# Kernel tuning notes

Measured on AMD Instinct MI355X. Metric: run time of the kernel, lower is better.

The kernel has to match this reference:

```python
import jax, jax.numpy as jnp
import numpy as np

B, S, D, H = 4, 2048, 1024, 16
DK = D // H


def setup_inputs() -> dict:
    key = jax.random.key(0)
    ks = jax.random.split(key, 12)
    s = 1.0 / np.sqrt(D)
    inp = {
        "query": jax.random.normal(ks[0], (B, S, D), jnp.float32),
        "key": jax.random.normal(ks[1], (B, S, D), jnp.float32),
        "value": jax.random.normal(ks[2], (B, S, D), jnp.float32),
        "mask": jax.random.randint(ks[3], (B, S, S), 0, 2, jnp.int32),
        "Wq": jax.random.uniform(ks[4], (D, D), jnp.float32, -s, s),
        "bq": jax.random.uniform(ks[5], (D,), jnp.float32, -s, s),
        "Wk": jax.random.uniform(ks[6], (D, D), jnp.float32, -s, s),
        "bk": jax.random.uniform(ks[7], (D,), jnp.float32, -s, s),
        "Wv": jax.random.uniform(ks[8], (D, D), jnp.float32, -s, s),
        "bv": jax.random.uniform(ks[9], (D,), jnp.float32, -s, s),
        "Wo": jax.random.uniform(ks[10], (D, D), jnp.float32, -s, s),
        "bo": jax.random.uniform(ks[11], (D,), jnp.float32, -s, s),
    }
    return inp


def reference(query, key, value, mask, Wq, bq, Wk, bk, Wv, bv, Wo, bo):
    # Linear projections (torch Linear: x @ W.T + b), split into heads: [B,H,S,DK]
    def proj(x, W, b):
        y = x @ W.T + b
        return y.reshape(B, S, H, DK).transpose(0, 2, 1, 3)

    q = proj(query, Wq, bq)
    k = proj(key, Wk, bk)
    v = proj(value, Wv, bv)

    # scores: [B,H,S,S]
    scores = jnp.einsum("bhqd,bhkd->bhqk", q, k) / jnp.sqrt(jnp.float32(DK))
    m = mask[:, None, :, :]  # broadcast over heads
    scores = jnp.where(m == 0, jnp.float32(-1e9), scores)
    attn = jax.nn.softmax(scores, axis=-1)
    out = jnp.einsum("bhqk,bhkd->bhqd", attn, v)
    out = out.transpose(0, 2, 1, 3).reshape(B, S, D)
    return out @ Wo.T + bo
```

## Files before the change

### kernel.cpp

```cpp
#include <hip/hip_runtime.h>

#define B_  4
#define S_  2048
#define D_  1024
#define H_  16
#define DK_ 64

typedef __attribute__((ext_vector_type(8))) __bf16 bf16x8;
typedef __attribute__((ext_vector_type(4))) float  f32x4;

#define AS1 __attribute__((address_space(1)))
#define AS3 __attribute__((address_space(3)))

__device__ __forceinline__ void gl2lds16(const void* g, void* l) {
    __builtin_amdgcn_global_load_lds((const AS1 unsigned int*)g,
                                     (AS3 unsigned int*)l, 16, 0, 0);
}

__device__ __forceinline__ unsigned short f2bf(float f) {
    union { float f; unsigned u; } v; v.f = f;
    return (unsigned short)((v.u + 0x7FFFu + ((v.u >> 16) & 1u)) >> 16);
}

__device__ __forceinline__ unsigned pk_bf16(float f0, float f1) {
    union { float f; unsigned u; } a, b; a.f = f0; b.f = f1;
    return __builtin_amdgcn_perm(b.u + 0x8000u, a.u + 0x8000u, 0x07060302u);
}

__device__ __forceinline__ void cast8(const float* __restrict__ x,
                                      unsigned short* __restrict__ y, int i) {
    float4 a = ((const float4*)x)[2 * i];
    float4 b = ((const float4*)x)[2 * i + 1];
    uint4 w;
    w.x = pk_bf16(a.x, a.y);
    w.y = pk_bf16(a.z, a.w);
    w.z = pk_bf16(b.x, b.y);
    w.w = pk_bf16(b.z, b.w);
    ((uint4*)y)[i] = w;
}

__global__ __launch_bounds__(256) void cast_act(
    const float* __restrict__ a, const float* __restrict__ b,
    const float* __restrict__ c, unsigned short* __restrict__ ya,
    unsigned short* __restrict__ yb, unsigned short* __restrict__ yc)
{
    const int sel = blockIdx.y;
    const float* x = (sel == 0) ? a : (sel == 1) ? b : c;
    unsigned short* y = (sel == 0) ? ya : (sel == 1) ? yb : yc;
    cast8(x, y, blockIdx.x * 256 + threadIdx.x);
}

__global__ __launch_bounds__(256) void cast_w(
    const float* __restrict__ a, const float* __restrict__ b,
    const float* __restrict__ c, const float* __restrict__ d,
    unsigned short* __restrict__ ya, unsigned short* __restrict__ yb,
    unsigned short* __restrict__ yc, unsigned short* __restrict__ yd)
{
    const int sel = blockIdx.y;
    const float* x = (sel == 0) ? a : (sel == 1) ? b : (sel == 2) ? c : d;
    unsigned short* y = (sel == 0) ? ya : (sel == 1) ? yb : (sel == 2) ? yc : yd;
    cast8(x, y, blockIdx.x * 256 + threadIdx.x);
}

__global__ __launch_bounds__(256, 3) void gemm_qkv(
    const unsigned short* __restrict__ Xq, const unsigned short* __restrict__ Xk,
    const unsigned short* __restrict__ Xv, const unsigned short* __restrict__ Wqkv,
    const float* __restrict__ bq, const float* __restrict__ bk,
    const float* __restrict__ bv, unsigned short* __restrict__ Qw,
    unsigned short* __restrict__ Kw, unsigned short* __restrict__ Vt,
    float qscale)
{
    __shared__ unsigned short As[128 * 64];
    __shared__ unsigned short Bs[128 * 64];

    const int tid  = threadIdx.x;
    const int lane = tid & 63, wave = tid >> 6;
    const int l16  = lane & 15, quad = lane >> 4;
    const int wm = wave & 1, wn = wave >> 1;
    const int n0 = blockIdx.x * 128, m0 = blockIdx.y * 128;
    const int xr = l16 & 7;

    const int sel = blockIdx.x >> 3;
    const unsigned short* X = (sel == 0) ? Xq : (sel == 1) ? Xk : Xv;

    const int row8 = lane >> 3;
    const int sc   = ((lane & 7) ^ row8) * 8;

    f32x4 acc[4][4] = {};

    for (int k0 = 0; k0 < D_; k0 += 64) {
        __syncthreads();
        #pragma unroll
        for (int j = 0; j < 4; ++j) {
            const int ca = wave * 4 + j;
            const int r  = ca * 8 + row8;
            gl2lds16(X    + (size_t)(m0 + r) * D_ + k0 + sc, &As[ca * 512 + (lane & 63) * 8]);
            gl2lds16(Wqkv + (size_t)(n0 + r) * D_ + k0 + sc, &Bs[ca * 512 + (lane & 63) * 8]);
        }
        __syncthreads();

        #pragma unroll
        for (int s = 0; s < 2; ++s) {
            bf16x8 a[4], bb[4];
            #pragma unroll
            for (int i = 0; i < 4; ++i)
                a[i] = *(const bf16x8*)&As[(wm * 64 + i * 16 + l16) * 64 + (((s * 4 + quad) ^ xr)) * 8];
            #pragma unroll
            for (int j = 0; j < 4; ++j)
                bb[j] = *(const bf16x8*)&Bs[(wn * 64 + j * 16 + l16) * 64 + (((s * 4 + quad) ^ xr)) * 8];
            #pragma unroll
            for (int i = 0; i < 4; ++i)
                #pragma unroll
                for (int j = 0; j < 4; ++j)
                    acc[i][j] = __builtin_amdgcn_mfma_f32_16x16x32_bf16(a[i], bb[j], acc[i][j], 0, 0, 0);
        }
    }

    const int ncol = (blockIdx.x & 7) * 128 + wn * 64;
    const float scale = (sel == 0) ? qscale : 1.0f;
    const float* bias = (sel == 0) ? bq : (sel == 1) ? bk : bv;

    if (sel == 2) {
        const int bb_ = m0 >> 11;
        #pragma unroll
        for (int j = 0; j < 4; ++j) {
            const int dk = ncol + j * 16 + l16;
            const float bvv = bias[dk];
            #pragma unroll
            for (int i = 0; i < 4; ++i) {
                const int sb = (m0 & (S_ - 1)) + wm * 64 + i * 16 + quad * 4;
                uint2 w;
                w.x = pk_bf16(acc[i][j][0] + bvv, acc[i][j][1] + bvv);
                w.y = pk_bf16(acc[i][j][2] + bvv, acc[i][j][3] + bvv);
                *(uint2*)(Vt + (size_t)(bb_ * D_ + dk) * S_ + sb) = w;
            }
        }
    } else {
        unsigned short* Outp = sel ? Kw : Qw;
        #pragma unroll
        for (int j = 0; j < 4; ++j) {
            const int n = ncol + j * 16 + l16;
            const float bvv = bias[n];
            #pragma unroll
            for (int i = 0; i < 4; ++i) {
                #pragma unroll
                for (int r = 0; r < 4; ++r) {
                    const int m = m0 + wm * 64 + i * 16 + quad * 4 + r;
                    Outp[(size_t)m * D_ + n] = f2bf((acc[i][j][r] + bvv) * scale);
                }
            }
        }
    }
}

__global__ __launch_bounds__(256, 3) void gemm_out(
    const unsigned short* __restrict__ X, const unsigned short* __restrict__ W,
    const float* __restrict__ bias, float* __restrict__ Out)
{
    __shared__ unsigned short As[128 * 64];
    __shared__ unsigned short Bs[128 * 64];

    const int tid  = threadIdx.x;
    const int lane = tid & 63, wave = tid >> 6;
    const int l16  = lane & 15, quad = lane >> 4;
    const int wm = wave & 1, wn = wave >> 1;
    const int n0 = blockIdx.x * 128, m0 = blockIdx.y * 128;
    const int xr = l16 & 7;

    const int row8 = lane >> 3;
    const int sc   = ((lane & 7) ^ row8) * 8;

    f32x4 acc[4][4] = {};

    for (int k0 = 0; k0 < D_; k0 += 64) {
        __syncthreads();
        #pragma unroll
        for (int j = 0; j < 4; ++j) {
            const int ca = wave * 4 + j;
            const int r  = ca * 8 + row8;
            gl2lds16(X + (size_t)(m0 + r) * D_ + k0 + sc, &As[ca * 512 + (lane & 63) * 8]);
            gl2lds16(W + (size_t)(n0 + r) * D_ + k0 + sc, &Bs[ca * 512 + (lane & 63) * 8]);
        }
        __syncthreads();

        #pragma unroll
        for (int s = 0; s < 2; ++s) {
            bf16x8 a[4], bb[4];
            #pragma unroll
            for (int i = 0; i < 4; ++i)
                a[i] = *(const bf16x8*)&As[(wm * 64 + i * 16 + l16) * 64 + (((s * 4 + quad) ^ xr)) * 8];
            #pragma unroll
            for (int j = 0; j < 4; ++j)
                bb[j] = *(const bf16x8*)&Bs[(wn * 64 + j * 16 + l16) * 64 + (((s * 4 + quad) ^ xr)) * 8];
            #pragma unroll
            for (int i = 0; i < 4; ++i)
                #pragma unroll
                for (int j = 0; j < 4; ++j)
                    acc[i][j] = __builtin_amdgcn_mfma_f32_16x16x32_bf16(a[i], bb[j], acc[i][j], 0, 0, 0);
        }
    }

    #pragma unroll
    for (int j = 0; j < 4; ++j) {
        const int n = n0 + wn * 64 + j * 16 + l16;
        const float bv = bias[n];
        #pragma unroll
        for (int i = 0; i < 4; ++i) {
            #pragma unroll
            for (int r = 0; r < 4; ++r) {
                const int m = m0 + wm * 64 + i * 16 + quad * 4 + r;
                Out[(size_t)m * D_ + n] = acc[i][j][r] + bv;
            }
        }
    }
}

__global__ __launch_bounds__(256) void pack_mask(
    const int* __restrict__ mask, unsigned long long* __restrict__ pm)
{
    const int gid  = blockIdx.x * 256 + threadIdx.x;
    const int w    = gid >> 6;
    const int lane = threadIdx.x & 63;
    const int mv = mask[(size_t)w * 64 + lane];
    const unsigned long long bal = __ballot(mv != 0);
    if (lane == 0) pm[w] = bal;
}

__global__ __launch_bounds__(256, 4) void attn_kernel(
    const unsigned short* __restrict__ Q,
    const unsigned short* __restrict__ Kg,
    const unsigned short* __restrict__ Vt,
    const unsigned long long* __restrict__ pm,
    unsigned short* __restrict__ O)
{
    __shared__ unsigned short Ks[64 * 64];
    __shared__ unsigned short VsT[80 * 64];
    __shared__ unsigned short Ps[64 * 72];

    const int tid  = threadIdx.x;
    const int lane = tid & 63, wave = tid >> 6;
    const int l16  = lane & 15, quad = lane >> 4;
    const int bh = blockIdx.y, b = bh >> 4, h = bh & 15;
    const int q0 = blockIdx.x * 64;
    const int xq = l16 & 7;

    {
        uint2 ones; ones.x = 0x3F803F80u; ones.y = 0x3F803F80u;
        *(uint2*)&VsT[64 * 64 + tid * 4] = ones;
    }

    bf16x8 qa[2];
    {
        const unsigned short* qp =
            Q + (size_t)(b * S_ + q0 + wave * 16 + l16) * D_ + h * DK_ + quad * 8;
        qa[0] = *(const bf16x8*)qp;
        qa[1] = *(const bf16x8*)(qp + 32);
    }

    const unsigned long long* pmq =
        pm + (size_t)(b * S_ + q0 + wave * 16 + l16) * (S_ / 64);

    f32x4 oacc[5] = {};

    for (int kt = 0; kt < S_ / 64; ++kt) {
        const int k0 = kt * 64;
        __syncthreads();
        #pragma unroll
        for (int j = 0; j < 2; ++j) {
            const int c = j * 256 + tid;
            const int row = c >> 3;
            const int cl = (c & 7) ^ (row & 7);
            gl2lds16(Kg + (size_t)(b * S_ + k0 + row) * D_ + h * DK_ + cl * 8, &Ks[c * 8]);
            gl2lds16(Vt + (size_t)(b * D_ + h * DK_ + row) * S_ + k0 + cl * 8, &VsT[c * 8]);
        }
        __syncthreads();

        f32x4 sct[4] = {};
        #pragma unroll
        for (int s = 0; s < 2; ++s) {
            const int cs = ((s * 4 + quad) ^ xq) * 8;
            #pragma unroll
            for (int mb = 0; mb < 4; ++mb) {
                bf16x8 ka = *(const bf16x8*)&Ks[(mb * 16 + l16) * 64 + cs];
                sct[mb] = __builtin_amdgcn_mfma_f32_16x16x32_bf16(ka, qa[s], sct[mb], 0, 0, 0);
            }
        }

        const unsigned long long wq = pmq[kt];
        #pragma unroll
        for (int mb = 0; mb < 4; ++mb) {
            const unsigned nib = (unsigned)(wq >> (mb * 16 + quad * 4)) & 0xFu;
            float e[4];
            #pragma unroll
            for (int r = 0; r < 4; ++r) {
                float x = __builtin_amdgcn_exp2f(sct[mb][r]);
                e[r] = ((nib >> r) & 1u) ? x : 0.f;
            }
            uint2 w;
            w.x = pk_bf16(e[0], e[1]);
            w.y = pk_bf16(e[2], e[3]);
            *(uint2*)&Ps[(wave * 16 + l16) * 72 + mb * 16 + quad * 4] = w;
        }

        #pragma unroll
        for (int s = 0; s < 2; ++s) {
            bf16x8 pa = *(const bf16x8*)&Ps[(wave * 16 + l16) * 72 + s * 32 + quad * 8];
            const int cs = ((s * 4 + quad) ^ xq) * 8;
            #pragma unroll
            for (int db = 0; db < 5; ++db) {
                bf16x8 vb = *(const bf16x8*)&VsT[(db * 16 + l16) * 64 + cs];
                oacc[db] = __builtin_amdgcn_mfma_f32_16x16x32_bf16(pa, vb, oacc[db], 0, 0, 0);
            }
        }
    }

    #pragma unroll
    for (int r = 0; r < 4; ++r) {
        const float linv = 1.0f / oacc[4][r];
        const int qg = q0 + wave * 16 + quad * 4 + r;
        #pragma unroll
        for (int db = 0; db < 4; ++db) {
            O[(size_t)(b * S_ + qg) * D_ + h * DK_ + db * 16 + l16] =
                f2bf(oacc[db][r] * linv);
        }
    }
}

extern "C" void kernel_launch(void* const* d_in, const int* in_sizes, int n_in,
                              void* d_out, int out_size, void* d_ws, size_t ws_size,
                              hipStream_t stream)
{
    const float* q   = (const float*)d_in[0];
    const float* k   = (const float*)d_in[1];
    const float* v   = (const float*)d_in[2];
    const int* mask  = (const int*)d_in[3];
    const float* Wq  = (const float*)d_in[4];
    const float* bq  = (const float*)d_in[5];
    const float* Wk  = (const float*)d_in[6];
    const float* bk  = (const float*)d_in[7];
    const float* Wv  = (const float*)d_in[8];
    const float* bv  = (const float*)d_in[9];
    const float* Wo  = (const float*)d_in[10];
    const float* bo  = (const float*)d_in[11];

    const size_t MN = (size_t)B_ * S_ * D_;
    const size_t WN = (size_t)D_ * D_;
    unsigned short* qb  = (unsigned short*)d_ws;
    unsigned short* kb  = qb + MN;
    unsigned short* vb  = kb + MN;
    unsigned short* Qw  = vb + MN;
    unsigned short* Kw  = Qw + MN;
    unsigned short* Vt  = Kw + MN;
    unsigned short* wqb = Vt + MN;
    unsigned short* wkb = wqb + WN;
    unsigned short* wvb = wkb + WN;
    unsigned short* wob = wvb + WN;
    unsigned short* Ow  = qb;
    unsigned long long* pm = (unsigned long long*)d_out;

    dim3 blk(256);
    const int actBlocks = (int)(MN / 8 / 256);
    const int wBlocks   = (int)(WN / 8 / 256);

    pack_mask<<<(B_ * S_ * S_) / 256, blk, 0, stream>>>(mask, pm);

    cast_act<<<dim3(actBlocks, 3), blk, 0, stream>>>(q, k, v, qb, kb, vb);
    cast_w<<<dim3(wBlocks, 4), blk, 0, stream>>>(Wq, Wk, Wv, Wo, wqb, wkb, wvb, wob);

    const float qscale = 1.44269504088896341f * 0.125f;

    gemm_qkv<<<dim3(3 * D_ / 128, (B_ * S_) / 128), blk, 0, stream>>>(
        qb, kb, vb, wqb, bq, bk, bv, Qw, Kw, Vt, qscale);

    attn_kernel<<<dim3(S_ / 64, B_ * H_), blk, 0, stream>>>(Qw, Kw, Vt, pm, Ow);

    gemm_out<<<dim3(D_ / 128, (B_ * S_) / 128), blk, 0, stream>>>(
        Ow, wob, bo, (float*)d_out);
}
```

Baseline: 438.0 us.

## Double-buffer K/V tiles in attention kernel and overlap loads with MFMA

Adds ping-pong LDS buffers for K and V so the next tile's global-to-LDS loads are issued before computing on the current tile, and the loop keeps a single barrier per iteration instead of two. The ones-row used for the softmax denominator moves from LDS into a register constant. The P tile's padded stride is replaced by an XOR swizzle to avoid bank conflicts. s_setprio raises wave priority around the MFMA sections. LDS use grows with the double buffer, which may lower occupancy under the launch bound of 4 blocks.

```diff
diff --git a/kernel.cpp b/kernel.cpp
--- a/kernel.cpp
+++ b/kernel.cpp
@@ -233,9 +233,9 @@
     const unsigned long long* __restrict__ pm,
     unsigned short* __restrict__ O)
 {
-    __shared__ unsigned short Ks[64 * 64];
-    __shared__ unsigned short VsT[80 * 64];
-    __shared__ unsigned short Ps[64 * 72];
+    __shared__ unsigned short Ks[2][64 * 64];
+    __shared__ unsigned short Vs[2][64 * 64];
+    __shared__ unsigned short Ps[64 * 64];
 
     const int tid  = threadIdx.x;
     const int lane = tid & 63, wave = tid >> 6;
@@ -244,10 +244,9 @@
     const int q0 = blockIdx.x * 64;
     const int xq = l16 & 7;
 
-    {
-        uint2 ones; ones.x = 0x3F803F80u; ones.y = 0x3F803F80u;
-        *(uint2*)&VsT[64 * 64 + tid * 4] = ones;
-    }
+    union { uint4 u; bf16x8 v; } ones_u;
+    ones_u.u = make_uint4(0x3F803F80u, 0x3F803F80u, 0x3F803F80u, 0x3F803F80u);
+    const bf16x8 vb_ones = ones_u.v;
 
     bf16x8 qa[2];
     {
@@ -257,36 +256,47 @@
         qa[1] = *(const bf16x8*)(qp + 32);
     }
 
-    const unsigned long long* pmq =
-        pm + (size_t)(b * S_ + q0 + wave * 16 + l16) * (S_ / 64);
-
-    f32x4 oacc[5] = {};
-
-    for (int kt = 0; kt < S_ / 64; ++kt) {
+    const unsigned short* Kbase = Kg + (size_t)(b * S_) * D_ + h * DK_;
+    const unsigned short* Vbase = Vt + (size_t)(b * D_ + h * DK_) * S_;
+
+    auto stage = [&](int bi, int kt) {
         const int k0 = kt * 64;
-        __syncthreads();
         #pragma unroll
         for (int j = 0; j < 2; ++j) {
             const int c = j * 256 + tid;
             const int row = c >> 3;
             const int cl = (c & 7) ^ (row & 7);
-            gl2lds16(Kg + (size_t)(b * S_ + k0 + row) * D_ + h * DK_ + cl * 8, &Ks[c * 8]);
-            gl2lds16(Vt + (size_t)(b * D_ + h * DK_ + row) * S_ + k0 + cl * 8, &VsT[c * 8]);
-        }
-        __syncthreads();
+            gl2lds16(Kbase + (size_t)(k0 + row) * D_ + cl * 8, &Ks[bi][c * 8]);
+            gl2lds16(Vbase + (size_t)row * S_ + k0 + cl * 8, &Vs[bi][c * 8]);
+        }
+    };
+
+    const unsigned long long* pmq =
+        pm + (size_t)(b * S_ + q0 + wave * 16 + l16) * (S_ / 64);
+
+    f32x4 oacc[5] = {};
+
+    stage(0, 0);
+    __syncthreads();
+
+    int bi = 0;
+    for (int kt = 0; kt < S_ / 64; ++kt) {
+        const unsigned long long wq = pmq[kt];
+        if (kt + 1 < S_ / 64) stage(bi ^ 1, kt + 1);
 
         f32x4 sct[4] = {};
+        __builtin_amdgcn_s_setprio(1);
         #pragma unroll
         for (int s = 0; s < 2; ++s) {
             const int cs = ((s * 4 + quad) ^ xq) * 8;
             #pragma unroll
             for (int mb = 0; mb < 4; ++mb) {
-                bf16x8 ka = *(const bf16x8*)&Ks[(mb * 16 + l16) * 64 + cs];
+                bf16x8 ka = *(const bf16x8*)&Ks[bi][(mb * 16 + l16) * 64 + cs];
                 sct[mb] = __builtin_amdgcn_mfma_f32_16x16x32_bf16(ka, qa[s], sct[mb], 0, 0, 0);
             }
         }
-
-        const unsigned long long wq = pmq[kt];
+        __builtin_amdgcn_s_setprio(0);
+
         #pragma unroll
         for (int mb = 0; mb < 4; ++mb) {
             const unsigned nib = (unsigned)(wq >> (mb * 16 + quad * 4)) & 0xFu;
@@ -299,19 +309,25 @@
             uint2 w;
             w.x = pk_bf16(e[0], e[1]);
             w.y = pk_bf16(e[2], e[3]);
-            *(uint2*)&Ps[(wave * 16 + l16) * 72 + mb * 16 + quad * 4] = w;
-        }
-
+            *(uint2*)&Ps[(wave * 16 + l16) * 64 + ((mb * 16 + quad * 4) ^ (xq * 8))] = w;
+        }
+
+        __builtin_amdgcn_s_setprio(1);
         #pragma unroll
         for (int s = 0; s < 2; ++s) {
-            bf16x8 pa = *(const bf16x8*)&Ps[(wave * 16 + l16) * 72 + s * 32 + quad * 8];
+            bf16x8 pa = *(const bf16x8*)&Ps[(wave * 16 + l16) * 64 + ((s * 32 + quad * 8) ^ (xq * 8))];
             const int cs = ((s * 4 + quad) ^ xq) * 8;
             #pragma unroll
-            for (int db = 0; db < 5; ++db) {
-                bf16x8 vb = *(const bf16x8*)&VsT[(db * 16 + l16) * 64 + cs];
+            for (int db = 0; db < 4; ++db) {
+                bf16x8 vb = *(const bf16x8*)&Vs[bi][(db * 16 + l16) * 64 + cs];
                 oacc[db] = __builtin_amdgcn_mfma_f32_16x16x32_bf16(pa, vb, oacc[db], 0, 0, 0);
             }
-        }
+            oacc[4] = __builtin_amdgcn_mfma_f32_16x16x32_bf16(pa, vb_ones, oacc[4], 0, 0, 0);
+        }
+        __builtin_amdgcn_s_setprio(0);
+
+        __syncthreads();
+        bi ^= 1;
     }
 
     #pragma unroll
```

Measured after the change: 433.5 us. About the same (-1.0%).
